# Performance work log

Hardware: AMD Instinct MI355X
Metric: run time of the kernel (lower is better)

Reference implementation:

```python
import jax, jax.numpy as jnp
import numpy as np

N, C, T, V = 64, 64, 300, 25  # batch, channels, frames, joints
CO = 64
EPS = 1e-5


def setup_inputs() -> dict:
    key = jax.random.key(0)
    ks = jax.random.split(key, 5)
    x = jax.random.normal(ks[0], (N, C, T, V), dtype=jnp.float32)
    lin_w = jax.random.normal(ks[1], (C, CO), dtype=jnp.float32) * np.sqrt(1.0 / CO)
    lin_b = jnp.zeros((1, 1, CO), dtype=jnp.float32)
    feat_mask = jax.random.normal(ks[2], (1, V, C), dtype=jnp.float32) * 0.1
    bn_gamma = jnp.ones((V * CO,), dtype=jnp.float32)
    bn_beta = jnp.zeros((V * CO,), dtype=jnp.float32)
    shift_in = jax.random.randint(ks[3], (V * C,), 0, V * C, dtype=jnp.int32)
    shift_out = jax.random.randint(ks[4], (V * CO,), 0, V * CO, dtype=jnp.int32)
    return {"x": x, "lin_w": lin_w, "lin_b": lin_b, "feat_mask": feat_mask,
            "bn_gamma": bn_gamma, "bn_beta": bn_beta,
            "shift_in": shift_in, "shift_out": shift_out}


def reference(x, lin_w, lin_b, feat_mask, bn_gamma, bn_beta, shift_in, shift_out):
    n, c, t, v = x.shape
    co = lin_w.shape[1]
    # (N,C,T,V) -> (N*T, V*C)
    xt = jnp.transpose(x, (0, 2, 3, 1)).reshape(n * t, v * c)
    # shift-in gather along feature axis
    xs = jnp.take(xt, shift_in, axis=1).reshape(n * t, v, c)
    # learned feature mask (tanh + 1)
    xs = xs * (jnp.tanh(feat_mask) + 1.0)
    # small channel-mixing matmul + bias
    y = jnp.einsum('nvc,cd->nvd', xs, lin_w) + lin_b  # (N*T, V, CO)
    y = y.reshape(n * t, v * co)
    # shift-out gather
    y = jnp.take(y, shift_out, axis=1)
    # BatchNorm1d (training mode: batch statistics over N*T)
    mean = jnp.mean(y, axis=0)
    var = jnp.mean(jnp.square(y - mean), axis=0)
    y = (y - mean) * jax.lax.rsqrt(var + EPS) * bn_gamma + bn_beta
    # back to (N, CO, T, V), residual (in==out -> identity down), ReLU
    y = jnp.transpose(y.reshape(n, t, v, co), (0, 3, 1, 2))
    return jax.nn.relu(y + x)
```

## Files before the change

kernel.cpp:

```cpp
#include <hip/hip_runtime.h>

typedef __bf16 bf16x8 __attribute__((ext_vector_type(8)));
typedef float f32x4 __attribute__((ext_vector_type(4)));
typedef unsigned short u16;
typedef unsigned int u32;
typedef unsigned long long u64;
typedef u16 u16x8 __attribute__((ext_vector_type(8)));

#define TID ((int)threadIdx.x)

constexpr int Nn = 64, Tt = 300, Vv = 25;
constexpr int Fin = 1600;
constexpr int RowsT = 19200;
constexpr int TBR = 16;
constexpr int NTB = 19;
constexpr int NBLK = Nn * NTB;
constexpr int RAWE = 64 * TBR * Vv;
constexpr int YP = 21;
constexpr float EPSv = 1e-5f;

constexpr int WS_EPI   = 12800;
constexpr int WS_WV    = 25600;
constexpr int WS_COMBO = 33792;
constexpr int WS_PART  = 40192;
constexpr size_t WS_NEED = (size_t)WS_PART + (size_t)NBLK * 3200 * 4;

__device__ __forceinline__ u16 f2b(float f) {
  u32 u = __float_as_uint(f);
  return (u16)((u + 0x7fffu + ((u >> 16) & 1u)) >> 16);
}
__device__ __forceinline__ float b2f(u16 h) {
  return __uint_as_float(((u32)h) << 16);
}
__device__ __forceinline__ u64 pack4(float a, float b, float c, float d) {
  return (u64)f2b(a) | ((u64)f2b(b) << 16) | ((u64)f2b(c) << 32) | ((u64)f2b(d) << 48);
}

__device__ __forceinline__ void stage_raw(const float* __restrict__ x,
                                          int n, int t0, int validg, u16* raw) {
  const int base = n * 480000 + t0 * 25;
  if (validg == TBR * 25) {
    #pragma unroll
    for (int i = 0; i < 13; ++i) {
      int q = TID + i * 512;
      if (q < 6400) {
        int c = q / 100;
        int g4 = (q - c * 100) * 4;
        float4 xv = *reinterpret_cast<const float4*>(x + base + c * 7500 + g4);
        *reinterpret_cast<u64*>(raw + q * 4) = pack4(xv.x, xv.y, xv.z, xv.w);
      }
    }
  } else {
    #pragma unroll
    for (int i = 0; i < 13; ++i) {
      int q = TID + i * 512;
      if (q < 6400) {
        int c = q / 100;
        int g4 = (q - c * 100) * 4;
        float4 xv = make_float4(0.f, 0.f, 0.f, 0.f);
        if (g4 < validg)
          xv = *reinterpret_cast<const float4*>(x + base + c * 7500 + g4);
        *reinterpret_cast<u64*>(raw + q * 4) = pack4(xv.x, xv.y, xv.z, xv.w);
      }
    }
  }
}

__device__ __forceinline__ void load_bfr_g(const u16* __restrict__ wv, bf16x8 bfr[2][4]) {
  int l = TID & 63;
  #pragma unroll
  for (int ks = 0; ks < 2; ++ks)
    #pragma unroll
    for (int nt = 0; nt < 4; ++nt)
      bfr[ks][nt] = *reinterpret_cast<const bf16x8*>(wv + ((((ks << 2) | nt) << 9) + l * 8));
}

__device__ __forceinline__ bf16x8 build_a(const u16* raw, const u32* __restrict__ combo,
                                          int v, int ks, int t, int grp) {
  int jb = v * 64 + ks * 32 + grp * 8;
  bf16x8 a;
  #pragma unroll
  for (int i = 0; i < 8; ++i) {
    u32 cb = combo[jb + i];
    float m = __uint_as_float((cb & 0xffffu) << 16);
    float xv = b2f(raw[(cb >> 16) + t * 25]);
    a[i] = (__bf16)(xv * m);
  }
  return a;
}

__global__ void k_wv(const float* __restrict__ lin_w, const float* __restrict__ feat_mask,
                     const int* __restrict__ shift_in, float* __restrict__ wsum,
                     u16* __restrict__ wv, u32* __restrict__ combo_g) {
  int gid = blockIdx.x * 256 + TID;
  if (gid < 3200) wsum[gid] = 0.f;
  if (gid < Fin) {
    int s = shift_in[gid];
    u32 off = (u32)((s & 63) * 400 + (s >> 6));
    float m = tanhf(feat_mask[gid]) + 1.0f;
    combo_g[gid] = (off << 16) | (u32)f2b(m);
  }
  if (gid >= 2048 && gid < 2560) {
    int t = gid - 2048;
    int l = t & 63, nt = (t >> 6) & 3, ks = t >> 8;
    int c0 = ks * 32 + (l >> 4) * 8, d = nt * 16 + (l & 15);
    u16x8 o8;
    #pragma unroll
    for (int i = 0; i < 8; ++i) o8[i] = f2b(lin_w[(c0 + i) * 64 + d]);
    *reinterpret_cast<u16x8*>(wv + ((((ks << 2) | nt) << 9) + l * 8)) = o8;
  }
}

template <int ATOMIC>
__global__ __launch_bounds__(512, 6) void k_stats(
    const float* __restrict__ x, const u16* __restrict__ wv,
    const u32* __restrict__ combo_g, float* __restrict__ target)
{
  __shared__ __align__(16) u16 raw[RAWE];
  bf16x8 bfr[2][4];
  load_bfr_g(wv, bfr);

  int bid = blockIdx.x;
  int n = bid / NTB, tb = bid - n * NTB;
  int t0 = tb * TBR;
  int validg = min(TBR, Tt - t0) * 25;
  int w = TID >> 6, l = TID & 63;
  int t_lane = l & 15, grp = l >> 4;

  stage_raw(x, n, t0, validg, raw);
  __syncthreads();

  float* pb = target + (ATOMIC ? 0 : bid * 3200);
  #pragma unroll
  for (int k = 0; k < 4; ++k) {
    int v = w + 8 * k;
    if (v < Vv) {
      bf16x8 a0 = build_a(raw, combo_g, v, 0, t_lane, grp);
      bf16x8 a1 = build_a(raw, combo_g, v, 1, t_lane, grp);
      float pr[4], qr[4];
      #pragma unroll
      for (int nt = 0; nt < 4; ++nt) {
        f32x4 acc = {0.f, 0.f, 0.f, 0.f};
        acc = __builtin_amdgcn_mfma_f32_16x16x32_bf16(a0, bfr[0][nt], acc, 0, 0, 0);
        acc = __builtin_amdgcn_mfma_f32_16x16x32_bf16(a1, bfr[1][nt], acc, 0, 0, 0);
        float pp = acc[0] + acc[1] + acc[2] + acc[3];
        float qq = acc[0]*acc[0] + acc[1]*acc[1] + acc[2]*acc[2] + acc[3]*acc[3];
        pp += __shfl_xor(pp, 16); pp += __shfl_xor(pp, 32);
        qq += __shfl_xor(qq, 16); qq += __shfl_xor(qq, 32);
        pr[nt] = pp; qr[nt] = qq;
      }
      if (ATOMIC) {
        if ((l & 48) == 0) {
          #pragma unroll
          for (int nt = 0; nt < 4; ++nt) {
            int col = v * 64 + nt * 16 + t_lane;
            atomicAdd(&pb[col], pr[nt]);
            atomicAdd(&pb[1600 + col], qr[nt]);
          }
        }
      } else {
        float pv = (grp & 2) ? ((grp & 1) ? pr[3] : pr[2]) : ((grp & 1) ? pr[1] : pr[0]);
        float qv = (grp & 2) ? ((grp & 1) ? qr[3] : qr[2]) : ((grp & 1) ? qr[1] : qr[0]);
        pb[v * 64 + l] = pv;
        pb[1600 + v * 64 + l] = qv;
      }
    }
  }
}

__global__ __launch_bounds__(256) void k_red(const float* __restrict__ part,
                                             float* __restrict__ wsum) {
  __shared__ float red[16 * 17];
  int col0 = blockIdx.x * 16;
  int c = TID & 15, ch = TID >> 4;
  float s = 0.f;
  int r0 = ch * 76;
  #pragma unroll 4
  for (int i = 0; i < 76; ++i) s += part[(r0 + i) * 3200 + col0 + c];
  red[ch * 17 + c] = s;
  __syncthreads();
  if (TID < 16) {
    float t = 0.f;
    #pragma unroll
    for (int j = 0; j < 16; ++j) t += red[j * 17 + TID];
    wsum[col0 + TID] = t;
  }
}

__global__ void k_epi(const float* __restrict__ wsum, const float* __restrict__ gamma,
                      const float* __restrict__ beta, const int* __restrict__ shift_out,
                      u64* __restrict__ epi_g) {
  int k = blockIdx.x * 256 + TID;
  if (k >= Fin) return;
  int s2 = shift_out[k];
  float sm = wsum[s2] * (1.0f / RowsT);
  float sq = wsum[1600 + s2] * (1.0f / RowsT);
  float rstd = rsqrtf(fmaxf(sq - sm * sm, 0.f) + EPSv);
  float sc = gamma[k] * rstd;
  int d = k & 63, v = k >> 6;
  epi_g[d * 25 + v] = (u64)__float_as_uint(sc)
                    | ((u64)f2b(beta[k] - sm * sc) << 32)
                    | ((u64)(u32)(s2 * YP) << 48);
}

__global__ __launch_bounds__(512, 4) void k_main(
    const float* __restrict__ x, const u16* __restrict__ wv,
    const u32* __restrict__ combo_g, const u64* __restrict__ epi_g,
    float* __restrict__ out)
{
  __shared__ __align__(16) unsigned char smem[80000];
  u16* raw   = reinterpret_cast<u16*>(smem);
  u32* combo = reinterpret_cast<u32*>(smem + 51200);
  u16* ylds  = reinterpret_cast<u16*>(smem);
  u64* epi   = reinterpret_cast<u64*>(smem + 67200);

  int bid = blockIdx.x;
  int n = bid / NTB, tb = bid - n * NTB;
  int t0 = tb * TBR;
  int validg = min(TBR, Tt - t0) * 25;

  bf16x8 bfr[2][4];
  load_bfr_g(wv, bfr);
  stage_raw(x, n, t0, validg, raw);
  #pragma unroll
  for (int i = 0; i < 4; ++i) {
    int j = TID + i * 512;
    if (j < Fin) {
      combo[j] = combo_g[j];
      epi[j] = epi_g[j];
    }
  }
  __syncthreads();

  int w = TID >> 6, l = TID & 63, grp = l >> 4, t_lane = l & 15;
  bf16x8 areg[4][2];
  #pragma unroll
  for (int k = 0; k < 4; ++k) {
    int v = w + 8 * k;
    if (v < Vv) {
      areg[k][0] = build_a(raw, combo, v, 0, t_lane, grp);
      areg[k][1] = build_a(raw, combo, v, 1, t_lane, grp);
    }
  }
  __syncthreads();

  #pragma unroll
  for (int k = 0; k < 4; ++k) {
    int v = w + 8 * k;
    if (v < Vv) {
      #pragma unroll
      for (int nt = 0; nt < 4; ++nt) {
        f32x4 acc = {0.f, 0.f, 0.f, 0.f};
        acc = __builtin_amdgcn_mfma_f32_16x16x32_bf16(areg[k][0], bfr[0][nt], acc, 0, 0, 0);
        acc = __builtin_amdgcn_mfma_f32_16x16x32_bf16(areg[k][1], bfr[1][nt], acc, 0, 0, 0);
        int o = (v * 64 + nt * 16 + t_lane) * YP + grp * 4;
        #pragma unroll
        for (int j = 0; j < 4; ++j) ylds[o + j] = f2b(acc[j]);
      }
    }
  }
  __syncthreads();

  const int obase = n * 480000 + t0 * 25;
  #pragma unroll
  for (int it = 0; it < 13; ++it) {
    int g = TID + it * 512;
    if (g < 6400) {
      int d = g / 100;
      int f0 = (g - d * 100) * 4;
      if (f0 < validg) {
        const float4 xr = *reinterpret_cast<const float4*>(x + obase + d * 7500 + f0);
        float4 o;
        float* op = &o.x;
        const float* xp = &xr.x;
        #pragma unroll
        for (int e = 0; e < 4; ++e) {
          int f = f0 + e;
          int t = f / 25;
          int v = f - t * 25;
          u64 ep = epi[d * 25 + v];
          float sc = __uint_as_float((u32)ep);
          float of = b2f((u16)(ep >> 32));
          float y = b2f(ylds[(int)(ep >> 48) + t]);
          op[e] = fmaxf(fmaf(y, sc, of) + xp[e], 0.f);
        }
        *reinterpret_cast<float4*>(out + obase + d * 7500 + f0) = o;
      }
    }
  }
}

extern "C" void kernel_launch(void* const* d_in, const int* in_sizes, int n_in,
                              void* d_out, int out_size, void* d_ws, size_t ws_size,
                              hipStream_t stream) {
  (void)in_sizes; (void)n_in; (void)out_size;
  const float* x        = (const float*)d_in[0];
  const float* lin_w    = (const float*)d_in[1];
  const float* feat_mask= (const float*)d_in[3];
  const float* gamma    = (const float*)d_in[4];
  const float* beta     = (const float*)d_in[5];
  const int*   shift_in = (const int*)d_in[6];
  const int*   shift_out= (const int*)d_in[7];
  float* wsum   = (float*)d_ws;
  u64*   epi_g  = (u64*)((char*)d_ws + WS_EPI);
  u16*   wv     = (u16*)((char*)d_ws + WS_WV);
  u32*   combo_g= (u32*)((char*)d_ws + WS_COMBO);
  float* part   = (float*)((char*)d_ws + WS_PART);

  k_wv<<<13, 256, 0, stream>>>(lin_w, feat_mask, shift_in, wsum, wv, combo_g);
  if (ws_size >= WS_NEED) {
    k_stats<0><<<NBLK, 512, 0, stream>>>(x, wv, combo_g, part);
    k_red<<<200, 256, 0, stream>>>(part, wsum);
  } else {
    k_stats<1><<<NBLK, 512, 0, stream>>>(x, wv, combo_g, wsum);
  }
  k_epi  <<<7, 256, 0, stream>>>(wsum, gamma, beta, shift_out, epi_g);
  k_main <<<NBLK, 512, 0, stream>>>(x, wv, combo_g, epi_g, (float*)d_out);
}
```

Before: 111.5 us.

## Materialize bf16 matmul output in stats pass and reuse it in output pass

The stats kernel now writes the bf16 matmul result for each tile to workspace, and a new output kernel reads that tile back instead of re-gathering x and recomputing the MFMA matmul. This removes the recompute of the gather and matmul in the second pass, at the cost of about 62 MB of extra global writes and reads. It also needs more workspace, and it falls back to the old atomic/recompute path when the workspace is too small.

Result: slower. 128.0 us (+14.8%).

```diff
diff --git a/kernel.cpp b/kernel.cpp
--- a/kernel.cpp
+++ b/kernel.cpp
@@ -23,7 +23,9 @@
 constexpr int WS_WV    = 25600;
 constexpr int WS_COMBO = 33792;
 constexpr int WS_PART  = 40192;
-constexpr size_t WS_NEED = (size_t)WS_PART + (size_t)NBLK * 3200 * 4;
+constexpr size_t WS_YW   = (size_t)WS_PART + (size_t)NBLK * 3200 * 4;
+constexpr size_t WS_NEED_PART = WS_YW;
+constexpr size_t WS_NEED_FULL = WS_YW + (size_t)NBLK * 25600 * 2;
 
 __device__ __forceinline__ u16 f2b(float f) {
   u32 u = __float_as_uint(f);
@@ -111,10 +113,10 @@
   }
 }
 
-template <int ATOMIC>
-__global__ __launch_bounds__(512, 6) void k_stats(
+__global__ __launch_bounds__(512, 6) void k_y(
     const float* __restrict__ x, const u16* __restrict__ wv,
-    const u32* __restrict__ combo_g, float* __restrict__ target)
+    const u32* __restrict__ combo_g, float* __restrict__ part,
+    u16* __restrict__ yw)
 {
   __shared__ __align__(16) u16 raw[RAWE];
   bf16x8 bfr[2][4];
@@ -130,7 +132,8 @@
   stage_raw(x, n, t0, validg, raw);
   __syncthreads();
 
-  float* pb = target + (ATOMIC ? 0 : bid * 3200);
+  float* pb = part + bid * 3200;
+  u16*   ywt = yw + (size_t)bid * 25600;
   #pragma unroll
   for (int k = 0; k < 4; ++k) {
     int v = w + 8 * k;
@@ -143,26 +146,58 @@
         f32x4 acc = {0.f, 0.f, 0.f, 0.f};
         acc = __builtin_amdgcn_mfma_f32_16x16x32_bf16(a0, bfr[0][nt], acc, 0, 0, 0);
         acc = __builtin_amdgcn_mfma_f32_16x16x32_bf16(a1, bfr[1][nt], acc, 0, 0, 0);
+        int col = v * 64 + nt * 16 + t_lane;
+        *reinterpret_cast<u64*>(ywt + col * 16 + grp * 4) =
+            pack4(acc[0], acc[1], acc[2], acc[3]);
         float pp = acc[0] + acc[1] + acc[2] + acc[3];
         float qq = acc[0]*acc[0] + acc[1]*acc[1] + acc[2]*acc[2] + acc[3]*acc[3];
         pp += __shfl_xor(pp, 16); pp += __shfl_xor(pp, 32);
         qq += __shfl_xor(qq, 16); qq += __shfl_xor(qq, 32);
         pr[nt] = pp; qr[nt] = qq;
       }
-      if (ATOMIC) {
+      float pv = (grp & 2) ? ((grp & 1) ? pr[3] : pr[2]) : ((grp & 1) ? pr[1] : pr[0]);
+      float qv = (grp & 2) ? ((grp & 1) ? qr[3] : qr[2]) : ((grp & 1) ? qr[1] : qr[0]);
+      pb[v * 64 + l] = pv;
+      pb[1600 + v * 64 + l] = qv;
+    }
+  }
+}
+
+__global__ __launch_bounds__(512, 6) void k_stats_atomic(
+    const float* __restrict__ x, const u16* __restrict__ wv,
+    const u32* __restrict__ combo_g, float* __restrict__ target)
+{
+  __shared__ __align__(16) u16 raw[RAWE];
+  bf16x8 bfr[2][4];
+  load_bfr_g(wv, bfr);
+  int bid = blockIdx.x;
+  int n = bid / NTB, tb = bid - n * NTB;
+  int t0 = tb * TBR;
+  int validg = min(TBR, Tt - t0) * 25;
+  int w = TID >> 6, l = TID & 63;
+  int t_lane = l & 15, grp = l >> 4;
+  stage_raw(x, n, t0, validg, raw);
+  __syncthreads();
+  #pragma unroll
+  for (int k = 0; k < 4; ++k) {
+    int v = w + 8 * k;
+    if (v < Vv) {
+      bf16x8 a0 = build_a(raw, combo_g, v, 0, t_lane, grp);
+      bf16x8 a1 = build_a(raw, combo_g, v, 1, t_lane, grp);
+      #pragma unroll
+      for (int nt = 0; nt < 4; ++nt) {
+        f32x4 acc = {0.f, 0.f, 0.f, 0.f};
+        acc = __builtin_amdgcn_mfma_f32_16x16x32_bf16(a0, bfr[0][nt], acc, 0, 0, 0);
+        acc = __builtin_amdgcn_mfma_f32_16x16x32_bf16(a1, bfr[1][nt], acc, 0, 0, 0);
+        float pp = acc[0] + acc[1] + acc[2] + acc[3];
+        float qq = acc[0]*acc[0] + acc[1]*acc[1] + acc[2]*acc[2] + acc[3]*acc[3];
+        pp += __shfl_xor(pp, 16); pp += __shfl_xor(pp, 32);
+        qq += __shfl_xor(qq, 16); qq += __shfl_xor(qq, 32);
         if ((l & 48) == 0) {
-          #pragma unroll
-          for (int nt = 0; nt < 4; ++nt) {
-            int col = v * 64 + nt * 16 + t_lane;
-            atomicAdd(&pb[col], pr[nt]);
-            atomicAdd(&pb[1600 + col], qr[nt]);
-          }
+          int col = v * 64 + nt * 16 + t_lane;
+          atomicAdd(&target[col], pp);
+          atomicAdd(&target[1600 + col], qq);
         }
-      } else {
-        float pv = (grp & 2) ? ((grp & 1) ? pr[3] : pr[2]) : ((grp & 1) ? pr[1] : pr[0]);
-        float qv = (grp & 2) ? ((grp & 1) ? qr[3] : qr[2]) : ((grp & 1) ? qr[1] : qr[0]);
-        pb[v * 64 + l] = pv;
-        pb[1600 + v * 64 + l] = qv;
       }
     }
   }
@@ -200,10 +235,58 @@
   int d = k & 63, v = k >> 6;
   epi_g[d * 25 + v] = (u64)__float_as_uint(sc)
                     | ((u64)f2b(beta[k] - sm * sc) << 32)
-                    | ((u64)(u32)(s2 * YP) << 48);
-}
-
-__global__ __launch_bounds__(512, 4) void k_main(
+                    | ((u64)(u32)s2 << 48);
+}
+
+__global__ __launch_bounds__(512, 6) void k_out(
+    const float* __restrict__ x, const u16* __restrict__ yw,
+    const u64* __restrict__ epi_g, float* __restrict__ out)
+{
+  __shared__ __align__(16) u16 ysm[25600];
+  int bid = blockIdx.x;
+  int n = bid / NTB, tb = bid - n * NTB;
+  int t0 = tb * TBR;
+  int validg = min(TBR, Tt - t0) * 25;
+
+  const u16* ywt = yw + (size_t)bid * 25600;
+  #pragma unroll
+  for (int r = 0; r < 7; ++r) {
+    int c = TID + r * 512;
+    if (c < 3200)
+      *reinterpret_cast<uint4*>(&ysm[c * 8]) =
+          *reinterpret_cast<const uint4*>(ywt + c * 8);
+  }
+  __syncthreads();
+
+  const int obase = n * 480000 + t0 * 25;
+  for (int it = 0; it < 13; ++it) {
+    int g = TID + it * 512;
+    if (g < 6400) {
+      int d = g / 100;
+      int f0 = (g - d * 100) * 4;
+      if (f0 < validg) {
+        const float4 xr = *reinterpret_cast<const float4*>(x + obase + d * 7500 + f0);
+        float4 o;
+        float* op = &o.x;
+        const float* xp = &xr.x;
+        #pragma unroll
+        for (int e = 0; e < 4; ++e) {
+          int f = f0 + e;
+          int t = f / 25;
+          int v = f - t * 25;
+          u64 ep = epi_g[d * 25 + v];
+          float sc = __uint_as_float((u32)ep);
+          float of = b2f((u16)(ep >> 32));
+          float y = b2f(ysm[((int)(ep >> 48) << 4) + t]);
+          op[e] = fmaxf(fmaf(y, sc, of) + xp[e], 0.f);
+        }
+        *reinterpret_cast<float4*>(out + obase + d * 7500 + f0) = o;
+      }
+    }
+  }
+}
+
+__global__ __launch_bounds__(512, 4) void k_main_fb(
     const float* __restrict__ x, const u16* __restrict__ wv,
     const u32* __restrict__ combo_g, const u64* __restrict__ epi_g,
     float* __restrict__ out)
@@ -281,7 +364,7 @@
           u64 ep = epi[d * 25 + v];
           float sc = __uint_as_float((u32)ep);
           float of = b2f((u16)(ep >> 32));
-          float y = b2f(ylds[(int)(ep >> 48) + t]);
+          float y = b2f(ylds[(int)(ep >> 48) * YP + t]);
           op[e] = fmaxf(fmaf(y, sc, of) + xp[e], 0.f);
         }
         *reinterpret_cast<float4*>(out + obase + d * 7500 + f0) = o;
@@ -306,14 +389,17 @@
   u16*   wv     = (u16*)((char*)d_ws + WS_WV);
   u32*   combo_g= (u32*)((char*)d_ws + WS_COMBO);
   float* part   = (float*)((char*)d_ws + WS_PART);
+  u16*   yw     = (u16*)((char*)d_ws + WS_YW);
 
   k_wv<<<13, 256, 0, stream>>>(lin_w, feat_mask, shift_in, wsum, wv, combo_g);
-  if (ws_size >= WS_NEED) {
-    k_stats<0><<<NBLK, 512, 0, stream>>>(x, wv, combo_g, part);
+  if (ws_size >= WS_NEED_FULL) {
+    k_y  <<<NBLK, 512, 0, stream>>>(x, wv, combo_g, part, yw);
     k_red<<<200, 256, 0, stream>>>(part, wsum);
+    k_epi<<<7, 256, 0, stream>>>(wsum, gamma, beta, shift_out, epi_g);
+    k_out<<<NBLK, 512, 0, stream>>>(x, yw, epi_g, (float*)d_out);
   } else {
-    k_stats<1><<<NBLK, 512, 0, stream>>>(x, wv, combo_g, wsum);
-  }
-  k_epi  <<<7, 256, 0, stream>>>(wsum, gamma, beta, shift_out, epi_g);
-  k_main <<<NBLK, 512, 0, stream>>>(x, wv, combo_g, epi_g, (float*)d_out);
-}
+    k_stats_atomic<<<NBLK, 512, 0, stream>>>(x, wv, combo_g, wsum);
+    k_epi<<<7, 256, 0, stream>>>(wsum, gamma, beta, shift_out, epi_g);
+    k_main_fb<<<NBLK, 512, 0, stream>>>(x, wv, combo_g, epi_g, (float*)d_out);
+  }
+}
```

## Shrink k_main LDS by reading combo/epi tables from global and packing y stores

Applied to the files above, without the earlier changes.

k_main no longer copies the combo and epilogue tables into shared memory. It reads them directly from global (cache-resident) memory, which cuts shared memory from 80 KB to about 51 KB. The y tile stride changes from a padded 21 to 16, so each MFMA output can be written as one packed 64-bit store instead of four scalar stores. Launch bounds rise to 6 blocks per CU to use the freed LDS for occupancy. The risks are more LDS bank conflicts with the unpadded stride and extra global/cache latency on the gather-heavy epilogue reads.

After: 173.0 us. 55.1% more time.

```diff
diff --git a/kernel.cpp b/kernel.cpp
--- a/kernel.cpp
+++ b/kernel.cpp
@@ -16,14 +16,13 @@
 constexpr int NTB = 19;
 constexpr int NBLK = Nn * NTB;
 constexpr int RAWE = 64 * TBR * Vv;
-constexpr int YP = 21;
 constexpr float EPSv = 1e-5f;
 
 constexpr int WS_EPI   = 12800;
 constexpr int WS_WV    = 25600;
 constexpr int WS_COMBO = 33792;
 constexpr int WS_PART  = 40192;
-constexpr size_t WS_NEED = (size_t)WS_PART + (size_t)NBLK * 3200 * 4;
+constexpr size_t WS_NEED_PART = (size_t)WS_PART + (size_t)NBLK * 3200 * 4;
 
 __device__ __forceinline__ u16 f2b(float f) {
   u32 u = __float_as_uint(f);
@@ -200,19 +199,17 @@
   int d = k & 63, v = k >> 6;
   epi_g[d * 25 + v] = (u64)__float_as_uint(sc)
                     | ((u64)f2b(beta[k] - sm * sc) << 32)
-                    | ((u64)(u32)(s2 * YP) << 48);
-}
-
-__global__ __launch_bounds__(512, 4) void k_main(
+                    | ((u64)(u32)(s2 * 16) << 48);
+}
+
+__global__ __launch_bounds__(512, 6) void k_main(
     const float* __restrict__ x, const u16* __restrict__ wv,
     const u32* __restrict__ combo_g, const u64* __restrict__ epi_g,
     float* __restrict__ out)
 {
-  __shared__ __align__(16) unsigned char smem[80000];
-  u16* raw   = reinterpret_cast<u16*>(smem);
-  u32* combo = reinterpret_cast<u32*>(smem + 51200);
-  u16* ylds  = reinterpret_cast<u16*>(smem);
-  u64* epi   = reinterpret_cast<u64*>(smem + 67200);
+  __shared__ __align__(16) u16 smem[RAWE];
+  u16* raw  = smem;
+  u16* ylds = smem;
 
   int bid = blockIdx.x;
   int n = bid / NTB, tb = bid - n * NTB;
@@ -222,14 +219,6 @@
   bf16x8 bfr[2][4];
   load_bfr_g(wv, bfr);
   stage_raw(x, n, t0, validg, raw);
-  #pragma unroll
-  for (int i = 0; i < 4; ++i) {
-    int j = TID + i * 512;
-    if (j < Fin) {
-      combo[j] = combo_g[j];
-      epi[j] = epi_g[j];
-    }
-  }
   __syncthreads();
 
   int w = TID >> 6, l = TID & 63, grp = l >> 4, t_lane = l & 15;
@@ -238,8 +227,8 @@
   for (int k = 0; k < 4; ++k) {
     int v = w + 8 * k;
     if (v < Vv) {
-      areg[k][0] = build_a(raw, combo, v, 0, t_lane, grp);
-      areg[k][1] = build_a(raw, combo, v, 1, t_lane, grp);
+      areg[k][0] = build_a(raw, combo_g, v, 0, t_lane, grp);
+      areg[k][1] = build_a(raw, combo_g, v, 1, t_lane, grp);
     }
   }
   __syncthreads();
@@ -253,9 +242,8 @@
         f32x4 acc = {0.f, 0.f, 0.f, 0.f};
         acc = __builtin_amdgcn_mfma_f32_16x16x32_bf16(areg[k][0], bfr[0][nt], acc, 0, 0, 0);
         acc = __builtin_amdgcn_mfma_f32_16x16x32_bf16(areg[k][1], bfr[1][nt], acc, 0, 0, 0);
-        int o = (v * 64 + nt * 16 + t_lane) * YP + grp * 4;
-        #pragma unroll
-        for (int j = 0; j < 4; ++j) ylds[o + j] = f2b(acc[j]);
+        int o = ((v * 64 + nt * 16 + t_lane) << 4) + (grp << 2);
+        *reinterpret_cast<u64*>(ylds + o) = pack4(acc[0], acc[1], acc[2], acc[3]);
       }
     }
   }
@@ -278,7 +266,7 @@
           int f = f0 + e;
           int t = f / 25;
           int v = f - t * 25;
-          u64 ep = epi[d * 25 + v];
+          u64 ep = epi_g[d * 25 + v];
           float sc = __uint_as_float((u32)ep);
           float of = b2f((u16)(ep >> 32));
           float y = b2f(ylds[(int)(ep >> 48) + t]);
@@ -308,12 +296,12 @@
   float* part   = (float*)((char*)d_ws + WS_PART);
 
   k_wv<<<13, 256, 0, stream>>>(lin_w, feat_mask, shift_in, wsum, wv, combo_g);
-  if (ws_size >= WS_NEED) {
+  if (ws_size >= WS_NEED_PART) {
     k_stats<0><<<NBLK, 512, 0, stream>>>(x, wv, combo_g, part);
     k_red<<<200, 256, 0, stream>>>(part, wsum);
   } else {
     k_stats<1><<<NBLK, 512, 0, stream>>>(x, wv, combo_g, wsum);
   }
-  k_epi  <<<7, 256, 0, stream>>>(wsum, gamma, beta, shift_out, epi_g);
-  k_main <<<NBLK, 512, 0, stream>>>(x, wv, combo_g, epi_g, (float*)d_out);
-}
+  k_epi <<<7, 256, 0, stream>>>(wsum, gamma, beta, shift_out, epi_g);
+  k_main<<<NBLK, 512, 0, stream>>>(x, wv, combo_g, epi_g, (float*)d_out);
+}
```
